# Kernel tuning notes

Hardware: AMD Instinct MI355X
Metric: run time of the kernel (lower is better)

Reference implementation:

```python
import jax, jax.numpy as jnp
import numpy as np

B, S, D = 2, 2048, 1024   # batch, seq, in_shape
H, E = 16, 64             # num_heads, out_shape (per-head dim)

def setup_inputs() -> dict:
    key = jax.random.key(0)
    ks = jax.random.split(key, 5)
    x = jax.random.normal(ks[0], (B, S, D), dtype=jnp.float32)
    Wq = jax.random.normal(ks[1], (H, D, E), dtype=jnp.float32) * 0.02
    Wk = jax.random.normal(ks[2], (H, D, E), dtype=jnp.float32) * 0.02
    Wv = jax.random.normal(ks[3], (H, D, E), dtype=jnp.float32) * 0.02
    W = jax.random.normal(ks[4], (H * E, E), dtype=jnp.float32) * 0.02
    return {"x": x, "Wq": Wq, "Wk": Wk, "Wv": Wv, "W": W}

def reference(x, Wq, Wk, Wv, W):
    # Per-head projections (stacked over heads): [B,H,S,E]
    q = jnp.einsum("bsd,hde->bhse", x, Wq)
    k = jnp.einsum("bsd,hde->bhse", x, Wk)
    v = jnp.einsum("bsd,hde->bhse", x, Wv)
    scale = 1.0 / jnp.sqrt(jnp.float32(E))
    # Full causal scores [B,H,S,S] with -inf above diagonal (as in original)
    scores = jnp.einsum("bhse,bhte->bhst", q, k) * scale
    causal = jnp.tril(jnp.ones((S, S), dtype=bool))
    scores = jnp.where(causal, scores, -jnp.inf)
    attn = jax.nn.softmax(scores, axis=-1)
    ctx = jnp.einsum("bhst,bhte->bhse", attn, v)          # [B,H,S,E]
    # concat heads along last dim (head-major order matches tf.concat over list)
    ctx = jnp.transpose(ctx, (0, 2, 1, 3)).reshape(B, S, H * E)
    return ctx @ W                                         # [B,S,E]
```

## Files before the change

kernel.cpp:

```cpp
#include <hip/hip_runtime.h>
#include <hip/hip_bf16.h>
#include <cstdint>
#include <cstddef>

#define BB 2
#define SS 2048
#define DD 1024
#define HH 16
#define EE 64

typedef short bf16x8 __attribute__((ext_vector_type(8)));
typedef short s4 __attribute__((ext_vector_type(4)));
typedef float f32x4 __attribute__((ext_vector_type(4)));
typedef float float4v __attribute__((ext_vector_type(4)));
typedef unsigned int u32x2 __attribute__((ext_vector_type(2)));
typedef unsigned int u32x4 __attribute__((ext_vector_type(4)));

#define GLDS(gp, lp) __builtin_amdgcn_global_load_lds( \
    (const __attribute__((address_space(1))) void*)(gp), \
    (__attribute__((address_space(3))) void*)(lp), 16, 0, 0)

static __device__ __forceinline__ short f2bf(float f) {
    union { float f; uint32_t u; } v; v.f = f;
    uint32_t r = (v.u + 0x7fffu + ((v.u >> 16) & 1u)) >> 16;
    return (short)r;
}

static __device__ __forceinline__ uint32_t cvtpk(float a, float b) {
    uint32_t r;
    asm("v_cvt_pk_bf16_f32 %0, %1, %2" : "=v"(r) : "v"(a), "v"(b));
    return r;
}

__global__ __launch_bounds__(256) void prep_kernel(const float* __restrict__ x,
                                                   const float* __restrict__ Wq,
                                                   const float* __restrict__ Wk,
                                                   const float* __restrict__ Wv,
                                                   const float* __restrict__ W,
                                                   short* __restrict__ xb,
                                                   short* __restrict__ wt,
                                                   short* __restrict__ wot) {
    __shared__ float tile[64][65];
    int blk = blockIdx.x;
    int t = threadIdx.x;
    if (blk < 4096) {
        int i = blk * 256 + t;
        float4v v = ((const float4v*)x)[i];
        s4 o; o[0] = f2bf(v[0]); o[1] = f2bf(v[1]); o[2] = f2bf(v[2]); o[3] = f2bf(v[3]);
        ((s4*)xb)[i] = o;
        return;
    }
    int idx = blk - 4096;
    const float* src;
    short* d;
    int R, r0;
    if (idx < 768) {
        int bx = idx & 15, by = idx >> 4;
        int which = by >> 4, mtx = by & 15;
        src = ((which == 0) ? Wq : (which == 1) ? Wk : Wv) + (size_t)mtx * DD * 64;
        d = wt + (size_t)which * HH * EE * DD + (size_t)mtx * DD * 64;
        R = DD; r0 = bx * 64;
    } else {
        int bx = idx - 768;
        src = W; d = wot; R = HH * EE; r0 = bx * 64;
    }
#pragma unroll
    for (int i = 0; i < 16; ++i) {
        int id2 = t + i * 256;
        int r = id2 >> 6, c = id2 & 63;
        tile[r][c] = src[(size_t)(r0 + r) * 64 + c];
    }
    __syncthreads();
#pragma unroll
    for (int i = 0; i < 16; ++i) {
        int id2 = t + i * 256;
        int e = id2 >> 6, dd2 = id2 & 63;
        d[(size_t)e * R + r0 + dd2] = f2bf(tile[dd2][e]);
    }
}

__global__ __launch_bounds__(256, 3) void qkv_gemm(const short* __restrict__ A,
                                                   const short* __restrict__ Bt,
                                                   short* __restrict__ Qo,
                                                   short* __restrict__ Ko,
                                                   short* __restrict__ Vto) {
    __shared__ __align__(16) short As3[3][64 * 64];
    __shared__ __align__(16) short Bs3[3][64 * 64];
    int tid = threadIdx.x;
    int wv = tid >> 6, lane = tid & 63;
    int m = lane & 15, g = lane >> 4;
    int wr = wv >> 1, wc = wv & 1;

    int xcd = blockIdx.x & 7, idx = blockIdx.x >> 3;
    int mb = (xcd & 3) * 8 + (idx & 7);
    int nb = (xcd >> 2) * 12 + (idx >> 3);
    int rowBase = mb * 128, colBase0 = nb * 128;

    int src_row[2], src_kcol[2];
#pragma unroll
    for (int j = 0; j < 2; ++j) {
        int si = j * 256 + tid;
        int sr = si >> 3, sp = si & 7;
        int sl = sp ^ (sr & 7);
        src_row[j] = 2 * sr + (sl >> 2);
        src_kcol[j] = (sl & 3) * 8;
    }
    const short* aP0 = A + (size_t)(rowBase + src_row[0]) * DD + src_kcol[0];
    const short* aP1 = A + (size_t)(rowBase + src_row[1]) * DD + src_kcol[1];
    const short* bP0 = Bt + (size_t)(colBase0 + src_row[0]) * DD + src_kcol[0];
    const short* bP1 = Bt + (size_t)(colBase0 + src_row[1]) * DD + src_kcol[1];
    int dst0 = (wv * 64) * 8;
    int dst1 = (256 + wv * 64) * 8;

    f32x4 acc[4][4];
#pragma unroll
    for (int i = 0; i < 4; ++i)
#pragma unroll
        for (int j = 0; j < 4; ++j) acc[i][j] = {0, 0, 0, 0};

    int rdoff = ((m & 1) * 64 + g * 16) ^ (((m >> 1) & 7) << 4);
    int mh = m >> 1;

    auto STAGE = [&](int buf, int kt) {
        short* ab = &As3[buf][0];
        short* bb = &Bs3[buf][0];
        GLDS(aP0 + kt, ab + dst0);
        GLDS(aP1 + kt, ab + dst1);
        GLDS(bP0 + kt, bb + dst0);
        GLDS(bP1 + kt, bb + dst1);
    };

    auto COMPUTE = [&](int buf) {
        bf16x8 af[4], bfr[4];
#pragma unroll
        for (int mi = 0; mi < 4; ++mi)
            af[mi] = *(const bf16x8*)((const char*)&As3[buf][(wr * 32 + mi * 8 + mh) * 64] + rdoff);
#pragma unroll
        for (int ni = 0; ni < 4; ++ni)
            bfr[ni] = *(const bf16x8*)((const char*)&Bs3[buf][(wc * 32 + ni * 8 + mh) * 64] + rdoff);
        asm volatile("s_waitcnt lgkmcnt(0)\ns_barrier" ::: "memory");
        __builtin_amdgcn_s_setprio(1);
#pragma unroll
        for (int mi = 0; mi < 4; ++mi)
#pragma unroll
            for (int ni = 0; ni < 4; ++ni)
                acc[mi][ni] = __builtin_amdgcn_mfma_f32_16x16x32_bf16(af[mi], bfr[ni], acc[mi][ni], 0, 0, 0);
        __builtin_amdgcn_s_setprio(0);
    };

    STAGE(0, 0);
    STAGE(1, 32);
    for (int t = 0; t < 30; ++t) {
        STAGE((t + 2) % 3, (t + 2) * 32);
        asm volatile("s_waitcnt vmcnt(8)\ns_barrier" ::: "memory");
        COMPUTE(t % 3);
    }
    asm volatile("s_waitcnt vmcnt(4)\ns_barrier" ::: "memory");
    COMPUTE(0);
    asm volatile("s_waitcnt vmcnt(0)\ns_barrier" ::: "memory");
    COMPUTE(1);

    int colw = colBase0 + wc * 64;
    int mtx = colw >> 10;
    int h = (colw >> 6) & 15;
    int rb = rowBase + wr * 64;

    if (mtx == 0) {
        const float qs = 0.125f * 1.44269504089f;
#pragma unroll
        for (int mi = 0; mi < 4; ++mi)
#pragma unroll
            for (int ni = 0; ni < 4; ++ni)
#pragma unroll
                for (int r = 0; r < 4; ++r) {
                    int row = rb + mi * 16 + g * 4 + r;
                    int b = row >> 11, s = row & 2047;
                    Qo[((size_t)(b * HH + h) * SS + s) * EE + ni * 16 + m] = f2bf(acc[mi][ni][r] * qs);
                }
    } else if (mtx == 1) {
#pragma unroll
        for (int mi = 0; mi < 4; ++mi)
#pragma unroll
            for (int ni = 0; ni < 4; ++ni)
#pragma unroll
                for (int r = 0; r < 4; ++r) {
                    int row = rb + mi * 16 + g * 4 + r;
                    int b = row >> 11, s = row & 2047;
                    Ko[((size_t)(b * HH + h) * SS + s) * EE + ni * 16 + m] = f2bf(acc[mi][ni][r]);
                }
    } else {
#pragma unroll
        for (int mi = 0; mi < 4; ++mi)
#pragma unroll
            for (int ni = 0; ni < 4; ++ni) {
                int row0 = rb + mi * 16 + g * 4;
                int b = row0 >> 11, s = row0 & 2047;
                s4 o; o[0] = f2bf(acc[mi][ni][0]); o[1] = f2bf(acc[mi][ni][1]);
                o[2] = f2bf(acc[mi][ni][2]); o[3] = f2bf(acc[mi][ni][3]);
                *(s4*)&Vto[((size_t)(b * HH + h) * EE + ni * 16 + m) * SS + s] = o;
            }
    }
}

__global__ __launch_bounds__(256, 5) void attn_kernel(const short* __restrict__ Q,
                                                      const short* __restrict__ K,
                                                      const short* __restrict__ Vt,
                                                      short* __restrict__ ctx) {
    __shared__ __align__(16) short Ks[2][64 * 64];
    __shared__ __align__(16) short Vs[2][64 * 64];
    int tid = threadIdx.x;
    int wv = tid >> 6, lane = tid & 63;
    int m = lane & 15, g = lane >> 4;
    int xcd = blockIdx.x & 7, i = blockIdx.x >> 3;
    int bh = xcd * 4 + (i & 3);
    int qblk = 31 - (i >> 2);
    int b = bh >> 4, h = bh & 15;
    const short* Qb = Q + (size_t)bh * SS * EE;
    const short* Kb = K + (size_t)bh * SS * EE;
    const short* Vb = Vt + (size_t)bh * EE * SS;
    int qrow = qblk * 64 + wv * 16 + m;

    int srow = wv * 8 + (lane >> 3);
    int scol_s = (((lane & 7) * 16) ^ ((srow & 7) << 4)) >> 1;
    int trow = ((srow >> 4) & 1) * 32 + ((srow >> 2) & 3) * 8 + (srow & 3);

    bf16x8 qa0 = *(const bf16x8*)(Qb + (size_t)qrow * EE + g * 8);
    bf16x8 qa1 = *(const bf16x8*)(Qb + (size_t)qrow * EE + 32 + g * 8);

    int sw = (m & 7) << 4;
    int c0 = (g * 16) ^ sw;
    int c1 = (64 + g * 16) ^ sw;

    float mreg = -INFINITY, lsum = 0.f;
    f32x4 o[4];
#pragma unroll
    for (int n = 0; n < 4; ++n) { o[n][0] = 0.f; o[n][1] = 0.f; o[n][2] = 0.f; o[n][3] = 0.f; }

    auto STAGE = [&](int nb, int t0) {
        short* kd = &Ks[0][0] + nb * 4096 + wv * 512;
        short* vd = &Vs[0][0] + nb * 4096 + wv * 512;
        const short* ksrc = Kb + (size_t)(t0 + trow) * EE + scol_s;
        const short* vsrc = Vb + (size_t)srow * SS + t0 + scol_s;
        GLDS(ksrc, kd);
        GLDS(ksrc + 4 * EE, kd + 2048);
        GLDS(vsrc, vd);
        GLDS(vsrc + (size_t)32 * SS, vd + 2048);
    };

    int ntile = qblk + 1;
    STAGE(0, 0);
    __syncthreads();

    for (int tt = 0; tt < ntile; ++tt) {
        if (tt + 1 < ntile) STAGE((tt + 1) & 1, (tt + 1) * 64);
        int t0 = tt * 64;
        const short* Ksb = &Ks[0][0] + (tt & 1) * 4096;
        const short* Vsb = &Vs[0][0] + (tt & 1) * 4096;

        f32x4 sc[4] = {{0,0,0,0},{0,0,0,0},{0,0,0,0},{0,0,0,0}};
#pragma unroll
        for (int n = 0; n < 4; ++n) {
            const char* krow = (const char*)(Ksb + (n * 16 + m) * 64);
            bf16x8 kb0 = *(const bf16x8*)(krow + c0);
            sc[n] = __builtin_amdgcn_mfma_f32_16x16x32_bf16(kb0, qa0, sc[n], 0, 0, 0);
            bf16x8 kb1 = *(const bf16x8*)(krow + c1);
            sc[n] = __builtin_amdgcn_mfma_f32_16x16x32_bf16(kb1, qa1, sc[n], 0, 0, 0);
        }

        if (tt == qblk) {
#pragma unroll
            for (int n = 0; n < 4; ++n)
#pragma unroll
                for (int r = 0; r < 4; ++r) {
                    int t = t0 + 32 * (n & 1) + 8 * g + 4 * (n >> 1) + r;
                    if (t > qrow) sc[n][r] = -INFINITY;
                }
        }

        float mx = sc[0][0];
#pragma unroll
        for (int n = 0; n < 4; ++n)
#pragma unroll
            for (int r = 0; r < 4; ++r) mx = fmaxf(mx, sc[n][r]);
        mx = fmaxf(mx, __shfl_xor(mx, 16, 64));
        mx = fmaxf(mx, __shfl_xor(mx, 32, 64));

        if (!__all(mx <= mreg + 11.5f)) {
            float mn = fmaxf(mreg, mx);
            float al = exp2f(mreg - mn);
            lsum *= al;
#pragma unroll
            for (int n = 0; n < 4; ++n)
#pragma unroll
                for (int r = 0; r < 4; ++r) o[n][r] *= al;
            mreg = mn;
        }

#pragma unroll
        for (int n = 0; n < 4; ++n) {
            sc[n][0] = exp2f(sc[n][0] - mreg);
            sc[n][1] = exp2f(sc[n][1] - mreg);
            sc[n][2] = exp2f(sc[n][2] - mreg);
            sc[n][3] = exp2f(sc[n][3] - mreg);
            lsum += (sc[n][0] + sc[n][1]) + (sc[n][2] + sc[n][3]);
        }

#pragma unroll
        for (int ks = 0; ks < 2; ++ks) {
            union { u32x4 w; bf16x8 v; } pu;
            pu.w[0] = cvtpk(sc[ks][0], sc[ks][1]);
            pu.w[1] = cvtpk(sc[ks][2], sc[ks][3]);
            pu.w[2] = cvtpk(sc[ks + 2][0], sc[ks + 2][1]);
            pu.w[3] = cvtpk(sc[ks + 2][2], sc[ks + 2][3]);
            bf16x8 pa = pu.v;
            int cv = ks ? c1 : c0;
#pragma unroll
            for (int n = 0; n < 4; ++n) {
                const char* vrow = (const char*)(Vsb + (n * 16 + m) * 64);
                bf16x8 vb = *(const bf16x8*)(vrow + cv);
                o[n] = __builtin_amdgcn_mfma_f32_16x16x32_bf16(vb, pa, o[n], 0, 0, 0);
            }
        }

        __syncthreads();
    }

    lsum += __shfl_xor(lsum, 16, 64);
    lsum += __shfl_xor(lsum, 32, 64);
    float inv = 1.0f / lsum;
    short* cb = ctx + (size_t)(b * SS + qrow) * (HH * EE) + h * EE;
#pragma unroll
    for (int n = 0; n < 4; ++n) {
        u32x2 k0; k0[0] = cvtpk(o[n][0] * inv, o[n][1] * inv);
        k0[1] = cvtpk(o[n][2] * inv, o[n][3] * inv);
        *(u32x2*)&cb[n * 16 + g * 4] = k0;
    }
}

__global__ __launch_bounds__(256) void outproj_kernel(const short* __restrict__ ctx,
                                                      const short* __restrict__ wot,
                                                      float* __restrict__ out) {
    __shared__ float red[4][1024];
    int wv = threadIdx.x >> 6, lane = threadIdx.x & 63;
    int m = lane & 15, g = lane >> 4;
    int r0 = blockIdx.x * 16;
    const short* arow = ctx + (size_t)(r0 + m) * (HH * EE) + g * 8;
    const short* wb = wot + g * 8;
    f32x4 acc[4] = {{0,0,0,0},{0,0,0,0},{0,0,0,0},{0,0,0,0}};
    int k0 = wv * 256;
    for (int d0 = k0; d0 < k0 + 256; d0 += 32) {
        bf16x8 a = *(const bf16x8*)(arow + d0);
#pragma unroll
        for (int n = 0; n < 4; ++n) {
            bf16x8 bbf = *(const bf16x8*)(wb + (size_t)(n * 16 + m) * (HH * EE) + d0);
            acc[n] = __builtin_amdgcn_mfma_f32_16x16x32_bf16(a, bbf, acc[n], 0, 0, 0);
        }
    }
#pragma unroll
    for (int n = 0; n < 4; ++n)
#pragma unroll
        for (int r = 0; r < 4; ++r)
            red[wv][(g * 4 + r) * 64 + n * 16 + m] = acc[n][r];
    __syncthreads();
    int t = threadIdx.x;
    float4v sum = ((const float4v*)red[0])[t];
    sum += ((const float4v*)red[1])[t];
    sum += ((const float4v*)red[2])[t];
    sum += ((const float4v*)red[3])[t];
    ((float4v*)(out + (size_t)blockIdx.x * 1024))[t] = sum;
}

extern "C" void kernel_launch(void* const* d_in, const int* in_sizes, int n_in,
                              void* d_out, int out_size, void* d_ws, size_t ws_size,
                              hipStream_t stream) {
    const float* x  = (const float*)d_in[0];
    const float* Wq = (const float*)d_in[1];
    const float* Wk = (const float*)d_in[2];
    const float* Wv = (const float*)d_in[3];
    const float* W  = (const float*)d_in[4];
    float* out = (float*)d_out;

    char* w = (char*)d_ws;
    short* xb  = (short*)w;
    short* wqt = (short*)(w + ((size_t)8 << 20));
    short* wot = wqt + (size_t)3 * HH * EE * DD;
    short* Qb  = wot + (size_t)64 * 1024;
    short* Kb  = Qb + (size_t)BB * HH * SS * EE;
    short* Vtb = Kb + (size_t)BB * HH * SS * EE;
    short* ctx = Vtb + (size_t)BB * HH * SS * EE;

    prep_kernel<<<4880, 256, 0, stream>>>(x, Wq, Wk, Wv, W, xb, wqt, wot);
    qkv_gemm<<<768, 256, 0, stream>>>(xb, wqt, Qb, Kb, Vtb);
    attn_kernel<<<1024, 256, 0, stream>>>(Qb, Kb, Vtb, ctx);
    outproj_kernel<<<256, 256, 0, stream>>>(ctx, wot, out);
}
```

Measured before the change: 92.50 us.

## Split long causal query blocks across KV chunks and merge partials

Query blocks with many causal KV tiles are split into up to three chunks of at most 12 tiles each. A lookup table assigns (query block, chunk) pairs to the 1920 attention workgroups. Chunked blocks write unnormalized bf16 partial outputs plus per-row max and sum to scratch space, and a new merge kernel combines them with log-sum-exp rescaling. This targets the tail caused by the longest causal rows dominating attention time, at the cost of an extra kernel launch, extra scratch traffic and bf16 rounding of the partial outputs.

```diff
diff --git a/kernel.cpp b/kernel.cpp
--- a/kernel.cpp
+++ b/kernel.cpp
@@ -20,10 +20,27 @@
     (const __attribute__((address_space(1))) void*)(gp), \
     (__attribute__((address_space(3))) void*)(lp), 16, 0, 0)
 
+__device__ const unsigned char QTAB[60] = {
+    11,12,13,14,15,16,17,18,19,20,21,22,23, 24,25,26,27,28,29,30,31,
+    24,25,26,27,28,29,30,31, 23,
+    10,22,  9,21,  8,20,
+     7,19,31,  6,18,30,  5,17,29,  4,16,28,
+     3,15,27,  2,14,26,  1,13,25,  0,12,24 };
+__device__ const unsigned char CTAB[60] = {
+     0, 0, 0, 0, 0, 0, 0, 0, 0, 0, 0, 0, 0,  0, 0, 0, 0, 0, 0, 0, 0,
+     1, 1, 1, 1, 1, 1, 1, 1,  1,
+     0, 1,  0, 1,  0, 1,
+     0, 1, 2,  0, 1, 2,  0, 1, 2,  0, 1, 2,
+     0, 1, 2,  0, 1, 2,  0, 1, 2,  0, 1, 2 };
+
 static __device__ __forceinline__ short f2bf(float f) {
     union { float f; uint32_t u; } v; v.f = f;
     uint32_t r = (v.u + 0x7fffu + ((v.u >> 16) & 1u)) >> 16;
     return (short)r;
+}
+static __device__ __forceinline__ float bf2f(short s) {
+    union { uint32_t u; float f; } v; v.u = ((uint32_t)(unsigned short)s) << 16;
+    return v.f;
 }
 
 static __device__ __forceinline__ uint32_t cvtpk(float a, float b) {
@@ -205,7 +222,9 @@
 __global__ __launch_bounds__(256, 5) void attn_kernel(const short* __restrict__ Q,
                                                       const short* __restrict__ K,
                                                       const short* __restrict__ Vt,
-                                                      short* __restrict__ ctx) {
+                                                      short* __restrict__ ctx,
+                                                      short* __restrict__ po,
+                                                      float* __restrict__ pml) {
     __shared__ __align__(16) short Ks[2][64 * 64];
     __shared__ __align__(16) short Vs[2][64 * 64];
     int tid = threadIdx.x;
@@ -213,7 +232,11 @@
     int m = lane & 15, g = lane >> 4;
     int xcd = blockIdx.x & 7, i = blockIdx.x >> 3;
     int bh = xcd * 4 + (i & 3);
-    int qblk = 31 - (i >> 2);
+    int entry = i >> 2;
+    int qblk = QTAB[entry], ch = CTAB[entry];
+    int nc = (qblk < 12) ? 1 : (qblk < 24 ? 2 : 3);
+    int tc0 = ch * 12;
+    int tc1 = min(qblk, tc0 + 11);
     int b = bh >> 4, h = bh & 15;
     const short* Qb = Q + (size_t)bh * SS * EE;
     const short* Kb = K + (size_t)bh * SS * EE;
@@ -247,13 +270,14 @@
         GLDS(vsrc + (size_t)32 * SS, vd + 2048);
     };
 
-    int ntile = qblk + 1;
-    STAGE(0, 0);
+    int ntile = tc1 - tc0 + 1;
+    STAGE(0, tc0 * 64);
     __syncthreads();
 
     for (int tt = 0; tt < ntile; ++tt) {
-        if (tt + 1 < ntile) STAGE((tt + 1) & 1, (tt + 1) * 64);
-        int t0 = tt * 64;
+        int tabs = tc0 + tt;
+        if (tt + 1 < ntile) STAGE((tt + 1) & 1, (tabs + 1) * 64);
+        int t0 = tabs * 64;
         const short* Ksb = &Ks[0][0] + (tt & 1) * 4096;
         const short* Vsb = &Vs[0][0] + (tt & 1) * 4096;
 
@@ -267,7 +291,7 @@
             sc[n] = __builtin_amdgcn_mfma_f32_16x16x32_bf16(kb1, qa1, sc[n], 0, 0, 0);
         }
 
-        if (tt == qblk) {
+        if (tabs == qblk) {
 #pragma unroll
             for (int n = 0; n < 4; ++n)
 #pragma unroll
@@ -327,14 +351,58 @@
 
     lsum += __shfl_xor(lsum, 16, 64);
     lsum += __shfl_xor(lsum, 32, 64);
-    float inv = 1.0f / lsum;
-    short* cb = ctx + (size_t)(b * SS + qrow) * (HH * EE) + h * EE;
-#pragma unroll
-    for (int n = 0; n < 4; ++n) {
-        u32x2 k0; k0[0] = cvtpk(o[n][0] * inv, o[n][1] * inv);
-        k0[1] = cvtpk(o[n][2] * inv, o[n][3] * inv);
-        *(u32x2*)&cb[n * 16 + g * 4] = k0;
-    }
+
+    if (nc == 1) {
+        float inv = 1.0f / lsum;
+        short* cb = ctx + (size_t)(b * SS + qrow) * (HH * EE) + h * EE;
+#pragma unroll
+        for (int n = 0; n < 4; ++n) {
+            u32x2 k0; k0[0] = cvtpk(o[n][0] * inv, o[n][1] * inv);
+            k0[1] = cvtpk(o[n][2] * inv, o[n][3] * inv);
+            *(u32x2*)&cb[n * 16 + g * 4] = k0;
+        }
+    } else {
+        int sl = bh * 48 + ((qblk < 24) ? (qblk - 12) * 2 + ch : 24 + (qblk - 24) * 3 + ch);
+        int row = wv * 16 + m;
+        short* od = po + (size_t)sl * 4096 + row * 64;
+#pragma unroll
+        for (int n = 0; n < 4; ++n) {
+            u32x2 k0; k0[0] = cvtpk(o[n][0], o[n][1]);
+            k0[1] = cvtpk(o[n][2], o[n][3]);
+            *(u32x2*)&od[n * 16 + g * 4] = k0;
+        }
+        if (g == 0) {
+            pml[(size_t)sl * 128 + row] = mreg;
+            pml[(size_t)sl * 128 + 64 + row] = lsum;
+        }
+    }
+}
+
+__global__ __launch_bounds__(256) void merge_kernel(const short* __restrict__ po,
+                                                    const float* __restrict__ pml,
+                                                    short* __restrict__ ctx) {
+    int wv = threadIdx.x >> 6, e = threadIdx.x & 63;
+    int rid = blockIdx.x * 4 + wv;
+    int bh = rid / 1280, rem = rid % 1280;
+    int q = 12 + (rem >> 6), row = rem & 63;
+    int nc = (q < 24) ? 2 : 3;
+    int s0 = bh * 48 + ((q < 24) ? (q - 12) * 2 : 24 + (q - 24) * 3);
+
+    float mm[3], ll[3];
+    float M = -INFINITY;
+    for (int c = 0; c < nc; ++c) {
+        mm[c] = pml[(size_t)(s0 + c) * 128 + row];
+        ll[c] = pml[(size_t)(s0 + c) * 128 + 64 + row];
+        M = fmaxf(M, mm[c]);
+    }
+    float osum = 0.f, lt = 0.f;
+    for (int c = 0; c < nc; ++c) {
+        float scv = exp2f(mm[c] - M);
+        lt += scv * ll[c];
+        osum += scv * bf2f(po[(size_t)(s0 + c) * 4096 + row * 64 + e]);
+    }
+    int b = bh >> 4, h = bh & 15;
+    ctx[(size_t)(b * SS + q * 64 + row) * (HH * EE) + h * EE + e] = f2bf(osum / lt);
 }
 
 __global__ __launch_bounds__(256) void outproj_kernel(const short* __restrict__ ctx,
@@ -389,8 +457,12 @@
     short* Vtb = Kb + (size_t)BB * HH * SS * EE;
     short* ctx = Vtb + (size_t)BB * HH * SS * EE;
 
+    short* part_o  = (short*)w;
+    float* part_ml = (float*)(w + 12582912);
+
     prep_kernel<<<4880, 256, 0, stream>>>(x, Wq, Wk, Wv, W, xb, wqt, wot);
     qkv_gemm<<<768, 256, 0, stream>>>(xb, wqt, Qb, Kb, Vtb);
-    attn_kernel<<<1024, 256, 0, stream>>>(Qb, Kb, Vtb, ctx);
+    attn_kernel<<<1920, 256, 0, stream>>>(Qb, Kb, Vtb, ctx, part_o, part_ml);
+    merge_kernel<<<10240, 256, 0, stream>>>(part_o, part_ml, ctx);
     outproj_kernel<<<256, 256, 0, stream>>>(ctx, wot, out);
 }
```

After: 99.98 us. 8.1% more time.
